# Kernel optimization log

Hardware: AMD Instinct MI355X
Metric: run time of the kernel (lower is better)

## Reference

```python
import jax, jax.numpy as jnp
import numpy as np

N_NODES = 20000
N_EDGES = 320000
DIM_IN = 768
DIM_H = 512
S_HOPS = 3
NUM_GNNS = 4
NEG_SLOPE = 0.2  # DGL GATConv default


def setup_inputs() -> dict:
    key = jax.random.key(0)
    ks = jax.random.split(key, 12)
    feat = jax.random.normal(ks[0], (N_NODES, DIM_IN), dtype=jnp.float32)
    src = jax.random.randint(ks[1], (N_EDGES,), 0, N_NODES)
    dst = jax.random.randint(ks[2], (N_EDGES,), 0, N_NODES)
    # learned params
    fc_W = jax.random.normal(ks[3], (DIM_IN, DIM_H), dtype=jnp.float32) * 0.02
    fc_b = jnp.zeros((DIM_H,), dtype=jnp.float32)
    gat_W = jax.random.normal(ks[4], (NUM_GNNS, DIM_H, DIM_H), dtype=jnp.float32) * 0.02
    gat_al = jax.random.normal(ks[5], (NUM_GNNS, DIM_H), dtype=jnp.float32) * 0.1
    gat_ar = jax.random.normal(ks[6], (NUM_GNNS, DIM_H), dtype=jnp.float32) * 0.1
    gat_b = jnp.zeros((NUM_GNNS, DIM_H), dtype=jnp.float32)
    beta = jnp.ones((S_HOPS + 1,), dtype=jnp.float32)
    return {"feat": feat, "fc_W": fc_W, "fc_b": fc_b, "gat_W": gat_W,
            "gat_al": gat_al, "gat_ar": gat_ar, "gat_b": gat_b,
            "beta": beta, "src": src, "dst": dst}


def _gat_layer(h, W, a_l, a_r, b, src, dst):
    z = h @ W                                   # [N, DH]
    el = z @ a_l                                # [N]
    er = z @ a_r                                # [N]
    e = jax.nn.leaky_relu(el[src] + er[dst], NEG_SLOPE)  # [E]
    # edge softmax over incoming edges of each dst node
    m = jax.ops.segment_max(e, dst, num_segments=N_NODES)
    ex = jnp.exp(e - m[dst])
    denom = jax.ops.segment_sum(ex, dst, num_segments=N_NODES)
    alpha = ex / denom[dst]                     # [E]
    out = jax.ops.segment_sum(alpha[:, None] * z[src], dst, num_segments=N_NODES)
    return out + b


def reference(feat, fc_W, fc_b, gat_W, gat_al, gat_ar, gat_b, beta, src, dst):
    h = feat @ fc_W + fc_b                      # dim_in -> 512
    for l in range(NUM_GNNS):
        h = _gat_layer(h, gat_W[l], gat_al[l], gat_ar[l], gat_b[l], src, dst)
    # A_hat = A + I propagation; A_hat @ Z = scatter(Z[src] -> dst) + Z
    Z_prev = h
    Z = beta[0] * Z_prev                        # accumulated Z is computed but the
    for s in range(1, S_HOPS + 1):              # original module returns Z_prev
        Z_s = jax.ops.segment_sum(Z_prev[src], dst, num_segments=N_NODES) + Z_prev
        Z = Z + beta[s] * Z_s
        Z_prev = Z_s
    return Z_prev
```

## Files before the change

kernel.cpp:

```cpp
#include <hip/hip_runtime.h>
#include <math.h>

#define N_NODES 20000
#define M_PAD   20096
#define N_EDGES 320000
#define DIM_IN 768
#define DIM_H 512
#define NUM_GNNS 4
#define NEG_SLOPE 0.2f

#define GEMM_TILES 628
#define GEMM_GRID  632

typedef __attribute__((ext_vector_type(8))) short short8;
typedef __attribute__((ext_vector_type(4))) float f32x4;

#define GPTR(p) (const __attribute__((address_space(1))) void*)(p)
#define LPTR(p) (__attribute__((address_space(3))) void*)(p)

__device__ __forceinline__ float bf2f(unsigned int lo16) {
  return __uint_as_float(lo16 << 16);
}
__device__ __forceinline__ unsigned short f2bf(float f) {
  unsigned int u = __float_as_uint(f);
  u += 0x7FFFu + ((u >> 16) & 1u);
  return (unsigned short)(u >> 16);
}
__device__ __forceinline__ void unpack8(uint4 v, float* f) {
  f[0] = bf2f(v.x & 0xffffu); f[1] = bf2f(v.x >> 16);
  f[2] = bf2f(v.y & 0xffffu); f[3] = bf2f(v.y >> 16);
  f[4] = bf2f(v.z & 0xffffu); f[5] = bf2f(v.z >> 16);
  f[6] = bf2f(v.w & 0xffffu); f[7] = bf2f(v.w >> 16);
}
__device__ __forceinline__ uint4 pack8(const float* o) {
  uint4 pv;
  pv.x = (unsigned)f2bf(o[0]) | ((unsigned)f2bf(o[1]) << 16);
  pv.y = (unsigned)f2bf(o[2]) | ((unsigned)f2bf(o[3]) << 16);
  pv.z = (unsigned)f2bf(o[4]) | ((unsigned)f2bf(o[5]) << 16);
  pv.w = (unsigned)f2bf(o[6]) | ((unsigned)f2bf(o[7]) << 16);
  return pv;
}

__device__ __forceinline__ float waveReduceSum(float v) {
#pragma unroll
  for (int off = 32; off > 0; off >>= 1) v += __shfl_xor(v, off, 64);
  return v;
}
__device__ __forceinline__ float waveReduceMax(float v) {
#pragma unroll
  for (int off = 32; off > 0; off >>= 1) v = fmaxf(v, __shfl_xor(v, off, 64));
  return v;
}

__global__ __launch_bounds__(256) void gemm_mfma_bf16(
    const unsigned short* __restrict__ A,
    const unsigned short* __restrict__ Bt,
    const float* __restrict__ bias,
    unsigned short* __restrict__ Cbf,
    int K) {
  int bid = blockIdx.x;
  int tile = (bid & 7) * (GEMM_GRID / 8) + (bid >> 3);
  if (tile >= GEMM_TILES) return;
  int brow = tile >> 2;
  int bcol = tile & 3;

  __shared__ __align__(16) unsigned short As[128 * 32];
  __shared__ __align__(16) unsigned short Bs[128 * 32];
  int tid = threadIdx.x;
  int wave = tid >> 6, lane = tid & 63;
  int wm = wave >> 1, wn = wave & 1;

  int rl = lane >> 2;
  int kc = (lane & 3) ^ ((lane >> 3) & 3);
  int r0 = 32 * wave;
  const unsigned short* gA0 = A + (size_t)(brow * 128 + r0 + rl) * K + kc * 8;
  const unsigned short* gA1 = gA0 + (size_t)16 * K;
  const unsigned short* gB0 = Bt + (size_t)(bcol * 128 + r0 + rl) * K + kc * 8;
  const unsigned short* gB1 = gB0 + (size_t)16 * K;
  unsigned short* lA0 = As + r0 * 32;
  unsigned short* lA1 = As + (r0 + 16) * 32;
  unsigned short* lB0 = Bs + r0 * 32;
  unsigned short* lB1 = Bs + (r0 + 16) * 32;

  int mrow = lane & 15;
  int q = lane >> 4;
  int swz = (q ^ ((mrow >> 1) & 3)) * 8;
  const short8* ra = (const short8*)(As + (64 * wm + mrow) * 32 + swz);
  const short8* rb = (const short8*)(Bs + (64 * wn + mrow) * 32 + swz);

  f32x4 acc[4][4];
#pragma unroll
  for (int i = 0; i < 4; ++i)
#pragma unroll
    for (int j = 0; j < 4; ++j) acc[i][j] = (f32x4)(0.f);

  for (int k0 = 0; k0 < K; k0 += 32) {
    __syncthreads();
    __builtin_amdgcn_global_load_lds(GPTR(gA0 + k0), LPTR(lA0), 16, 0, 0);
    __builtin_amdgcn_global_load_lds(GPTR(gA1 + k0), LPTR(lA1), 16, 0, 0);
    __builtin_amdgcn_global_load_lds(GPTR(gB0 + k0), LPTR(lB0), 16, 0, 0);
    __builtin_amdgcn_global_load_lds(GPTR(gB1 + k0), LPTR(lB1), 16, 0, 0);
    __syncthreads();
    short8 a[4], b[4];
#pragma unroll
    for (int t = 0; t < 4; ++t) a[t] = ra[t * 64];
#pragma unroll
    for (int t = 0; t < 4; ++t) b[t] = rb[t * 64];
#pragma unroll
    for (int mt = 0; mt < 4; ++mt)
#pragma unroll
      for (int nt = 0; nt < 4; ++nt)
        acc[mt][nt] = __builtin_amdgcn_mfma_f32_16x16x32_bf16(a[mt], b[nt], acc[mt][nt], 0, 0, 0);
  }

  int colb = bcol * 128 + 64 * wn + (lane & 15);
  int rowb = brow * 128 + 64 * wm + 4 * q;
#pragma unroll
  for (int nt = 0; nt < 4; ++nt) {
    int col = colb + 16 * nt;
    float bv = bias ? bias[col] : 0.f;
#pragma unroll
    for (int mt = 0; mt < 4; ++mt) {
      int row = rowb + 16 * mt;
#pragma unroll
      for (int i = 0; i < 4; ++i)
        Cbf[(size_t)(row + i) * DIM_H + col] = f2bf(acc[mt][nt][i] + bv);
    }
  }
}

__global__ void convert_feat(const float* __restrict__ feat, unsigned short* __restrict__ Abf) {
  int t = blockIdx.x * blockDim.x + threadIdx.x;
  const int CHUNKS = M_PAD * DIM_IN / 8;
  if (t >= CHUNKS) return;
  int row = t / (DIM_IN / 8);
  uint4 o;
  if (row < N_NODES) {
    const float4* p = (const float4*)(feat + (size_t)t * 8);
    float4 x = p[0], y = p[1];
    o.x = (unsigned)f2bf(x.x) | ((unsigned)f2bf(x.y) << 16);
    o.y = (unsigned)f2bf(x.z) | ((unsigned)f2bf(x.w) << 16);
    o.z = (unsigned)f2bf(y.x) | ((unsigned)f2bf(y.y) << 16);
    o.w = (unsigned)f2bf(y.z) | ((unsigned)f2bf(y.w) << 16);
  } else {
    o = make_uint4(0, 0, 0, 0);
  }
  ((uint4*)Abf)[t] = o;
}

__global__ __launch_bounds__(256) void transpose_bf16(const float* __restrict__ in,
                                                      unsigned short* __restrict__ out,
                                                      int R, int C) {
  __shared__ float tile[32][33];
  int tx = threadIdx.x, ty = threadIdx.y;
  size_t base = (size_t)blockIdx.z * R * C;
  int r0 = blockIdx.x * 32, c0 = blockIdx.y * 32;
#pragma unroll
  for (int i = 0; i < 4; ++i) {
    int r = r0 + ty + i * 8;
    tile[ty + i * 8][tx] = in[base + (size_t)r * C + c0 + tx];
  }
  __syncthreads();
#pragma unroll
  for (int i = 0; i < 4; ++i) {
    int c = c0 + ty + i * 8;
    out[base + (size_t)c * R + r0 + tx] = f2bf(tile[tx][ty + i * 8]);
  }
}

__global__ void count_edges(const int* __restrict__ dst, int* __restrict__ counts) {
  int k = blockIdx.x * blockDim.x + threadIdx.x;
  if (k < N_EDGES) atomicAdd(&counts[dst[k]], 1);
}

__global__ __launch_bounds__(1024) void scan_kernel(const int* __restrict__ counts,
                                                    int* __restrict__ indptr) {
  __shared__ int part[1024];
  int tid = threadIdx.x;
  const int CH = (N_NODES + 1023) / 1024;
  int base = tid * CH;
  int s = 0;
  for (int i = 0; i < CH; ++i) {
    int idx = base + i;
    if (idx < N_NODES) s += counts[idx];
  }
  part[tid] = s;
  __syncthreads();
  for (int off = 1; off < 1024; off <<= 1) {
    int v = (tid >= off) ? part[tid - off] : 0;
    __syncthreads();
    part[tid] += v;
    __syncthreads();
  }
  int run = (tid == 0) ? 0 : part[tid - 1];
  for (int i = 0; i < CH; ++i) {
    int idx = base + i;
    if (idx < N_NODES) {
      indptr[idx] = run;
      run += counts[idx];
      if (idx == N_NODES - 1) indptr[N_NODES] = run;
    }
  }
}

__global__ void fill_adj(const int* __restrict__ src, const int* __restrict__ dst,
                         const int* __restrict__ indptr, int* __restrict__ cursor,
                         int* __restrict__ adjsrc) {
  int k = blockIdx.x * blockDim.x + threadIdx.x;
  if (k < N_EDGES) {
    int d = dst[k];
    int pos = atomicAdd(&cursor[d], 1);
    adjsrc[indptr[d] + pos] = src[k];
  }
}

__global__ __launch_bounds__(256) void eler_bf(const unsigned short* __restrict__ zbf,
                                               const float* __restrict__ al,
                                               const float* __restrict__ ar,
                                               float* __restrict__ el, float* __restrict__ er) {
  int wid = (blockIdx.x * blockDim.x + threadIdx.x) >> 6;
  int lane = threadIdx.x & 63;
  if (wid >= N_NODES) return;
  uint4 zv = ((const uint4*)(zbf + (size_t)wid * DIM_H))[lane];
  float z[8];
  unpack8(zv, z);
  const float4* al4 = (const float4*)(al + lane * 8);
  const float4* ar4 = (const float4*)(ar + lane * 8);
  float4 a0 = al4[0], a1 = al4[1], r0 = ar4[0], r1 = ar4[1];
  float sl = z[0] * a0.x + z[1] * a0.y + z[2] * a0.z + z[3] * a0.w +
             z[4] * a1.x + z[5] * a1.y + z[6] * a1.z + z[7] * a1.w;
  float sr = z[0] * r0.x + z[1] * r0.y + z[2] * r0.z + z[3] * r0.w +
             z[4] * r1.x + z[5] * r1.y + z[6] * r1.z + z[7] * r1.w;
  sl = waveReduceSum(sl);
  sr = waveReduceSum(sr);
  if (lane == 0) { el[wid] = sl; er[wid] = sr; }
}

__global__ __launch_bounds__(256) void gat_aggregate_bf(
    const unsigned short* __restrict__ zbf, const float* __restrict__ el,
    const float* __restrict__ er, const int* __restrict__ indptr,
    const int* __restrict__ adjsrc, const float* __restrict__ bias,
    unsigned short* __restrict__ out_bf) {
  int v = (blockIdx.x * blockDim.x + threadIdx.x) >> 6;
  int lane = threadIdx.x & 63;
  if (v >= N_NODES) return;
  int begin = indptr[v], end = indptr[v + 1];
  float er_v = er[v];

  float m = -INFINITY;
  for (int j = begin + lane; j < end; j += 64) {
    float e = el[adjsrc[j]] + er_v;
    e = (e >= 0.f) ? e : NEG_SLOPE * e;
    m = fmaxf(m, e);
  }
  m = waveReduceMax(m);

  float ssum = 0.f;
  for (int j = begin + lane; j < end; j += 64) {
    float e = el[adjsrc[j]] + er_v;
    e = (e >= 0.f) ? e : NEG_SLOPE * e;
    ssum += __expf(e - m);
  }
  float denom = waveReduceSum(ssum);
  float inv = (end > begin) ? 1.f / denom : 0.f;

  float acc[8] = {};
  for (int c = begin; c < end; c += 64) {
    int cc = min(64, end - c);
    int has = (c + lane < end);
    int sIdx = has ? adjsrc[c + lane] : 0;
    float e = has ? el[sIdx] + er_v : 0.f;
    e = (e >= 0.f) ? e : NEG_SLOPE * e;
    float wl = has ? __expf(e - m) * inv : 0.f;
    int t = 0;
    for (; t + 4 <= cc; t += 4) {
      int s0 = __shfl(sIdx, t + 0), s1 = __shfl(sIdx, t + 1);
      int s2 = __shfl(sIdx, t + 2), s3 = __shfl(sIdx, t + 3);
      float w0 = __shfl(wl, t + 0), w1 = __shfl(wl, t + 1);
      float w2 = __shfl(wl, t + 2), w3 = __shfl(wl, t + 3);
      uint4 z0 = ((const uint4*)(zbf + (size_t)s0 * DIM_H))[lane];
      uint4 z1 = ((const uint4*)(zbf + (size_t)s1 * DIM_H))[lane];
      uint4 z2 = ((const uint4*)(zbf + (size_t)s2 * DIM_H))[lane];
      uint4 z3 = ((const uint4*)(zbf + (size_t)s3 * DIM_H))[lane];
      float f0[8], f1[8], f2[8], f3[8];
      unpack8(z0, f0); unpack8(z1, f1); unpack8(z2, f2); unpack8(z3, f3);
#pragma unroll
      for (int i = 0; i < 8; ++i)
        acc[i] += w0 * f0[i] + w1 * f1[i] + w2 * f2[i] + w3 * f3[i];
    }
    for (; t < cc; ++t) {
      int s0 = __shfl(sIdx, t);
      float w0 = __shfl(wl, t);
      uint4 z0 = ((const uint4*)(zbf + (size_t)s0 * DIM_H))[lane];
      float f0[8];
      unpack8(z0, f0);
#pragma unroll
      for (int i = 0; i < 8; ++i) acc[i] += w0 * f0[i];
    }
  }
  const float4* b4 = (const float4*)(bias + lane * 8);
  float4 b0 = b4[0], b1 = b4[1];
  float o[8] = {acc[0] + b0.x, acc[1] + b0.y, acc[2] + b0.z, acc[3] + b0.w,
                acc[4] + b1.x, acc[5] + b1.y, acc[6] + b1.z, acc[7] + b1.w};
  ((uint4*)(out_bf + (size_t)v * DIM_H))[lane] = pack8(o);
}

__global__ __launch_bounds__(256) void propagate_bf(const unsigned short* __restrict__ zin,
                                                    const int* __restrict__ indptr,
                                                    const int* __restrict__ adjsrc,
                                                    unsigned short* __restrict__ out_bf,
                                                    float* __restrict__ out_f32) {
  int v = (blockIdx.x * blockDim.x + threadIdx.x) >> 6;
  int lane = threadIdx.x & 63;
  if (v >= N_NODES) return;
  uint4 sv = ((const uint4*)(zin + (size_t)v * DIM_H))[lane];
  float acc[8];
  unpack8(sv, acc);
  int begin = indptr[v], end = indptr[v + 1];
  for (int c = begin; c < end; c += 64) {
    int cc = min(64, end - c);
    int sIdx = (c + lane < end) ? adjsrc[c + lane] : 0;
    int t = 0;
    for (; t + 4 <= cc; t += 4) {
      int s0 = __shfl(sIdx, t + 0), s1 = __shfl(sIdx, t + 1);
      int s2 = __shfl(sIdx, t + 2), s3 = __shfl(sIdx, t + 3);
      uint4 z0 = ((const uint4*)(zin + (size_t)s0 * DIM_H))[lane];
      uint4 z1 = ((const uint4*)(zin + (size_t)s1 * DIM_H))[lane];
      uint4 z2 = ((const uint4*)(zin + (size_t)s2 * DIM_H))[lane];
      uint4 z3 = ((const uint4*)(zin + (size_t)s3 * DIM_H))[lane];
      float f0[8], f1[8], f2[8], f3[8];
      unpack8(z0, f0); unpack8(z1, f1); unpack8(z2, f2); unpack8(z3, f3);
#pragma unroll
      for (int i = 0; i < 8; ++i) acc[i] += f0[i] + f1[i] + f2[i] + f3[i];
    }
    for (; t < cc; ++t) {
      int s0 = __shfl(sIdx, t);
      uint4 z0 = ((const uint4*)(zin + (size_t)s0 * DIM_H))[lane];
      float f0[8];
      unpack8(z0, f0);
#pragma unroll
      for (int i = 0; i < 8; ++i) acc[i] += f0[i];
    }
  }
  if (out_bf) {
    ((uint4*)(out_bf + (size_t)v * DIM_H))[lane] = pack8(acc);
  } else {
    float4* fr = (float4*)(out_f32 + (size_t)v * DIM_H + lane * 8);
    fr[0] = make_float4(acc[0], acc[1], acc[2], acc[3]);
    fr[1] = make_float4(acc[4], acc[5], acc[6], acc[7]);
  }
}

extern "C" void kernel_launch(void* const* d_in, const int* in_sizes, int n_in,
                              void* d_out, int out_size, void* d_ws, size_t ws_size,
                              hipStream_t stream) {
  const float* feat = (const float*)d_in[0];
  const float* fc_W = (const float*)d_in[1];
  const float* fc_b = (const float*)d_in[2];
  const float* gat_W = (const float*)d_in[3];
  const float* gat_al = (const float*)d_in[4];
  const float* gat_ar = (const float*)d_in[5];
  const float* gat_b = (const float*)d_in[6];
  const int* src = (const int*)d_in[8];
  const int* dst = (const int*)d_in[9];
  float* out = (float*)d_out;

  char* w = (char*)d_ws;
  auto alloc = [&](size_t bytes) {
    char* p = w;
    w += (bytes + 255) & ~(size_t)255;
    return p;
  };
  unsigned short* hbf   = (unsigned short*)alloc((size_t)M_PAD * DIM_H * 2);
  unsigned short* fcWt  = (unsigned short*)alloc((size_t)DIM_H * DIM_IN * 2);
  unsigned short* gatWt = (unsigned short*)alloc((size_t)NUM_GNNS * DIM_H * DIM_H * 2);
  float* el    = (float*)alloc((size_t)N_NODES * 4);
  float* er    = (float*)alloc((size_t)N_NODES * 4);
  int* counts  = (int*)alloc((size_t)2 * N_NODES * 4);
  int* cursor  = counts + N_NODES;
  int* indptr  = (int*)alloc((size_t)(N_NODES + 1) * 4);
  int* adjsrc  = (int*)alloc((size_t)N_EDGES * 4);
  char* uni = alloc((size_t)M_PAD * DIM_IN * 2);
  unsigned short* Abf = (unsigned short*)uni;
  unsigned short* Z1  = (unsigned short*)uni;
  unsigned short* zbf = (unsigned short*)d_out;

  hipMemsetAsync(counts, 0, sizeof(int) * 2 * N_NODES, stream);
  count_edges<<<(N_EDGES + 255) / 256, 256, 0, stream>>>(dst, counts);
  scan_kernel<<<1, 1024, 0, stream>>>(counts, indptr);
  fill_adj<<<(N_EDGES + 255) / 256, 256, 0, stream>>>(src, dst, indptr, cursor, adjsrc);

  convert_feat<<<(M_PAD * DIM_IN / 8 + 255) / 256, 256, 0, stream>>>(feat, Abf);
  transpose_bf16<<<dim3(DIM_IN / 32, DIM_H / 32, 1), dim3(32, 8), 0, stream>>>(fc_W, fcWt, DIM_IN, DIM_H);
  transpose_bf16<<<dim3(DIM_H / 32, DIM_H / 32, NUM_GNNS), dim3(32, 8), 0, stream>>>(gat_W, gatWt, DIM_H, DIM_H);

  gemm_mfma_bf16<<<GEMM_GRID, 256, 0, stream>>>(Abf, fcWt, fc_b, hbf, DIM_IN);

  int nwaveblocks = (N_NODES * 64 + 255) / 256;
  for (int l = 0; l < NUM_GNNS; ++l) {
    gemm_mfma_bf16<<<GEMM_GRID, 256, 0, stream>>>(hbf, gatWt + (size_t)l * DIM_H * DIM_H,
                                                  nullptr, zbf, DIM_H);
    eler_bf<<<nwaveblocks, 256, 0, stream>>>(zbf, gat_al + (size_t)l * DIM_H,
                                             gat_ar + (size_t)l * DIM_H, el, er);
    gat_aggregate_bf<<<nwaveblocks, 256, 0, stream>>>(
        zbf, el, er, indptr, adjsrc, gat_b + (size_t)l * DIM_H, hbf);
  }

  propagate_bf<<<nwaveblocks, 256, 0, stream>>>(hbf, indptr, adjsrc, Z1, nullptr);
  propagate_bf<<<nwaveblocks, 256, 0, stream>>>(Z1, indptr, adjsrc, hbf, nullptr);
  propagate_bf<<<nwaveblocks, 256, 0, stream>>>(hbf, indptr, adjsrc, nullptr, out);
}
```

Baseline: 636.5 us.

## Slice gather aggregation by column blocks and precompute edge softmax weights

Splits the GAT edge softmax into its own kernel that writes per-edge alpha to a buffer, then aggregates and propagates with a column-sliced layout. Each block now owns one 64-column slice of 4 nodes, and its 4 lane-groups each handle a different edge before a cross-slot shuffle reduction. Grouping blocks by slice is meant to improve cache locality of the gathered rows and raise parallelism for each node. In exchange it launches an extra kernel per layer, launches 8x more blocks, and makes smaller 8-byte gathers.

```diff
diff --git a/kernel.cpp b/kernel.cpp
--- a/kernel.cpp
+++ b/kernel.cpp
@@ -11,6 +11,9 @@
 
 #define GEMM_TILES 628
 #define GEMM_GRID  632
+
+#define NODE_WAVE_BLOCKS 5000
+#define SLICED_GRID (NODE_WAVE_BLOCKS * 8)
 
 typedef __attribute__((ext_vector_type(8))) short short8;
 typedef __attribute__((ext_vector_type(4))) float f32x4;
@@ -236,11 +239,10 @@
   if (lane == 0) { el[wid] = sl; er[wid] = sr; }
 }
 
-__global__ __launch_bounds__(256) void gat_aggregate_bf(
-    const unsigned short* __restrict__ zbf, const float* __restrict__ el,
-    const float* __restrict__ er, const int* __restrict__ indptr,
-    const int* __restrict__ adjsrc, const float* __restrict__ bias,
-    unsigned short* __restrict__ out_bf) {
+__global__ __launch_bounds__(256) void edge_softmax_alpha(
+    const float* __restrict__ el, const float* __restrict__ er,
+    const int* __restrict__ indptr, const int* __restrict__ adjsrc,
+    float* __restrict__ alpha) {
   int v = (blockIdx.x * blockDim.x + threadIdx.x) >> 6;
   int lane = threadIdx.x & 63;
   if (v >= N_NODES) return;
@@ -255,99 +257,142 @@
   }
   m = waveReduceMax(m);
 
-  float ssum = 0.f;
+  float ss = 0.f;
   for (int j = begin + lane; j < end; j += 64) {
     float e = el[adjsrc[j]] + er_v;
     e = (e >= 0.f) ? e : NEG_SLOPE * e;
-    ssum += __expf(e - m);
-  }
-  float denom = waveReduceSum(ssum);
+    ss += __expf(e - m);
+  }
+  float denom = waveReduceSum(ss);
   float inv = (end > begin) ? 1.f / denom : 0.f;
 
-  float acc[8] = {};
+  for (int j = begin + lane; j < end; j += 64) {
+    float e = el[adjsrc[j]] + er_v;
+    e = (e >= 0.f) ? e : NEG_SLOPE * e;
+    alpha[j] = __expf(e - m) * inv;
+  }
+}
+
+__global__ __launch_bounds__(256) void gat_aggregate_sliced(
+    const unsigned short* __restrict__ zbf, const float* __restrict__ alpha,
+    const int* __restrict__ indptr, const int* __restrict__ adjsrc,
+    const float* __restrict__ bias, unsigned short* __restrict__ out_bf) {
+  int slice = blockIdx.x & 7;
+  int group = blockIdx.x >> 3;
+  int wave = threadIdx.x >> 6, lane = threadIdx.x & 63;
+  int v = group * 4 + wave;
+  if (v >= N_NODES) return;
+  int slot = lane >> 4, sub = lane & 15;
+  int col = slice * 64 + sub * 4;
+  const unsigned short* zc = zbf + col;
+
+  int begin = indptr[v], end = indptr[v + 1];
+  float acc[4] = {0.f, 0.f, 0.f, 0.f};
+
   for (int c = begin; c < end; c += 64) {
     int cc = min(64, end - c);
-    int has = (c + lane < end);
-    int sIdx = has ? adjsrc[c + lane] : 0;
-    float e = has ? el[sIdx] + er_v : 0.f;
-    e = (e >= 0.f) ? e : NEG_SLOPE * e;
-    float wl = has ? __expf(e - m) * inv : 0.f;
+    bool has = (c + lane < end);
+    int idx = has ? adjsrc[c + lane] : 0;
+    float wv = has ? alpha[c + lane] : 0.f;
     int t = 0;
-    for (; t + 4 <= cc; t += 4) {
-      int s0 = __shfl(sIdx, t + 0), s1 = __shfl(sIdx, t + 1);
-      int s2 = __shfl(sIdx, t + 2), s3 = __shfl(sIdx, t + 3);
-      float w0 = __shfl(wl, t + 0), w1 = __shfl(wl, t + 1);
-      float w2 = __shfl(wl, t + 2), w3 = __shfl(wl, t + 3);
-      uint4 z0 = ((const uint4*)(zbf + (size_t)s0 * DIM_H))[lane];
-      uint4 z1 = ((const uint4*)(zbf + (size_t)s1 * DIM_H))[lane];
-      uint4 z2 = ((const uint4*)(zbf + (size_t)s2 * DIM_H))[lane];
-      uint4 z3 = ((const uint4*)(zbf + (size_t)s3 * DIM_H))[lane];
-      float f0[8], f1[8], f2[8], f3[8];
-      unpack8(z0, f0); unpack8(z1, f1); unpack8(z2, f2); unpack8(z3, f3);
-#pragma unroll
-      for (int i = 0; i < 8; ++i)
-        acc[i] += w0 * f0[i] + w1 * f1[i] + w2 * f2[i] + w3 * f3[i];
-    }
-    for (; t < cc; ++t) {
-      int s0 = __shfl(sIdx, t);
-      float w0 = __shfl(wl, t);
-      uint4 z0 = ((const uint4*)(zbf + (size_t)s0 * DIM_H))[lane];
-      float f0[8];
-      unpack8(z0, f0);
-#pragma unroll
-      for (int i = 0; i < 8; ++i) acc[i] += w0 * f0[i];
-    }
-  }
-  const float4* b4 = (const float4*)(bias + lane * 8);
-  float4 b0 = b4[0], b1 = b4[1];
-  float o[8] = {acc[0] + b0.x, acc[1] + b0.y, acc[2] + b0.z, acc[3] + b0.w,
-                acc[4] + b1.x, acc[5] + b1.y, acc[6] + b1.z, acc[7] + b1.w};
-  ((uint4*)(out_bf + (size_t)v * DIM_H))[lane] = pack8(o);
-}
-
-__global__ __launch_bounds__(256) void propagate_bf(const unsigned short* __restrict__ zin,
-                                                    const int* __restrict__ indptr,
-                                                    const int* __restrict__ adjsrc,
-                                                    unsigned short* __restrict__ out_bf,
-                                                    float* __restrict__ out_f32) {
-  int v = (blockIdx.x * blockDim.x + threadIdx.x) >> 6;
-  int lane = threadIdx.x & 63;
+    for (; (t + 2) * 4 <= cc; t += 2) {
+      int e0 = t * 4 + slot, e1 = e0 + 4;
+      int s0 = __shfl(idx, e0, 64), s1 = __shfl(idx, e1, 64);
+      float w0 = __shfl(wv, e0, 64), w1 = __shfl(wv, e1, 64);
+      uint2 z0 = *(const uint2*)(zc + (size_t)s0 * DIM_H);
+      uint2 z1 = *(const uint2*)(zc + (size_t)s1 * DIM_H);
+      acc[0] += w0 * bf2f(z0.x & 0xffffu) + w1 * bf2f(z1.x & 0xffffu);
+      acc[1] += w0 * bf2f(z0.x >> 16)     + w1 * bf2f(z1.x >> 16);
+      acc[2] += w0 * bf2f(z0.y & 0xffffu) + w1 * bf2f(z1.y & 0xffffu);
+      acc[3] += w0 * bf2f(z0.y >> 16)     + w1 * bf2f(z1.y >> 16);
+    }
+    for (; t * 4 < cc; ++t) {
+      int e0 = t * 4 + slot;
+      int s0 = __shfl(idx, e0, 64);
+      float w0 = __shfl(wv, e0, 64);
+      uint2 z0 = *(const uint2*)(zc + (size_t)s0 * DIM_H);
+      acc[0] += w0 * bf2f(z0.x & 0xffffu);
+      acc[1] += w0 * bf2f(z0.x >> 16);
+      acc[2] += w0 * bf2f(z0.y & 0xffffu);
+      acc[3] += w0 * bf2f(z0.y >> 16);
+    }
+  }
+#pragma unroll
+  for (int i = 0; i < 4; ++i) {
+    acc[i] += __shfl_xor(acc[i], 16, 64);
+    acc[i] += __shfl_xor(acc[i], 32, 64);
+  }
+  if (slot == 0) {
+    float4 bv = *(const float4*)(bias + col);
+    unsigned long long pv =
+        (unsigned long long)((unsigned)f2bf(acc[0] + bv.x) | ((unsigned)f2bf(acc[1] + bv.y) << 16)) |
+        ((unsigned long long)((unsigned)f2bf(acc[2] + bv.z) | ((unsigned)f2bf(acc[3] + bv.w) << 16)) << 32);
+    __builtin_nontemporal_store(pv, (unsigned long long*)(out_bf + (size_t)v * DIM_H + col));
+  }
+}
+
+__global__ __launch_bounds__(256) void propagate_sliced(
+    const unsigned short* __restrict__ zin, const int* __restrict__ indptr,
+    const int* __restrict__ adjsrc, unsigned short* __restrict__ out_bf,
+    float* __restrict__ out_f32) {
+  int slice = blockIdx.x & 7;
+  int group = blockIdx.x >> 3;
+  int wave = threadIdx.x >> 6, lane = threadIdx.x & 63;
+  int v = group * 4 + wave;
   if (v >= N_NODES) return;
-  uint4 sv = ((const uint4*)(zin + (size_t)v * DIM_H))[lane];
-  float acc[8];
-  unpack8(sv, acc);
+  int slot = lane >> 4, sub = lane & 15;
+  int col = slice * 64 + sub * 4;
+  const unsigned short* zc = zin + col;
+
   int begin = indptr[v], end = indptr[v + 1];
+  float acc[4] = {0.f, 0.f, 0.f, 0.f};
+  if (slot == 0) {
+    uint2 sv = *(const uint2*)(zc + (size_t)v * DIM_H);
+    acc[0] = bf2f(sv.x & 0xffffu); acc[1] = bf2f(sv.x >> 16);
+    acc[2] = bf2f(sv.y & 0xffffu); acc[3] = bf2f(sv.y >> 16);
+  }
+
   for (int c = begin; c < end; c += 64) {
     int cc = min(64, end - c);
-    int sIdx = (c + lane < end) ? adjsrc[c + lane] : 0;
+    int idx = (c + lane < end) ? adjsrc[c + lane] : 0;
     int t = 0;
-    for (; t + 4 <= cc; t += 4) {
-      int s0 = __shfl(sIdx, t + 0), s1 = __shfl(sIdx, t + 1);
-      int s2 = __shfl(sIdx, t + 2), s3 = __shfl(sIdx, t + 3);
-      uint4 z0 = ((const uint4*)(zin + (size_t)s0 * DIM_H))[lane];
-      uint4 z1 = ((const uint4*)(zin + (size_t)s1 * DIM_H))[lane];
-      uint4 z2 = ((const uint4*)(zin + (size_t)s2 * DIM_H))[lane];
-      uint4 z3 = ((const uint4*)(zin + (size_t)s3 * DIM_H))[lane];
-      float f0[8], f1[8], f2[8], f3[8];
-      unpack8(z0, f0); unpack8(z1, f1); unpack8(z2, f2); unpack8(z3, f3);
-#pragma unroll
-      for (int i = 0; i < 8; ++i) acc[i] += f0[i] + f1[i] + f2[i] + f3[i];
-    }
-    for (; t < cc; ++t) {
-      int s0 = __shfl(sIdx, t);
-      uint4 z0 = ((const uint4*)(zin + (size_t)s0 * DIM_H))[lane];
-      float f0[8];
-      unpack8(z0, f0);
-#pragma unroll
-      for (int i = 0; i < 8; ++i) acc[i] += f0[i];
-    }
-  }
-  if (out_bf) {
-    ((uint4*)(out_bf + (size_t)v * DIM_H))[lane] = pack8(acc);
-  } else {
-    float4* fr = (float4*)(out_f32 + (size_t)v * DIM_H + lane * 8);
-    fr[0] = make_float4(acc[0], acc[1], acc[2], acc[3]);
-    fr[1] = make_float4(acc[4], acc[5], acc[6], acc[7]);
+    for (; (t + 2) * 4 <= cc; t += 2) {
+      int e0 = t * 4 + slot, e1 = e0 + 4;
+      int s0 = __shfl(idx, e0, 64), s1 = __shfl(idx, e1, 64);
+      uint2 z0 = *(const uint2*)(zc + (size_t)s0 * DIM_H);
+      uint2 z1 = *(const uint2*)(zc + (size_t)s1 * DIM_H);
+      acc[0] += bf2f(z0.x & 0xffffu) + bf2f(z1.x & 0xffffu);
+      acc[1] += bf2f(z0.x >> 16)     + bf2f(z1.x >> 16);
+      acc[2] += bf2f(z0.y & 0xffffu) + bf2f(z1.y & 0xffffu);
+      acc[3] += bf2f(z0.y >> 16)     + bf2f(z1.y >> 16);
+    }
+    for (; t * 4 < cc; ++t) {
+      int e0 = t * 4 + slot;
+      int s0 = __shfl(idx, e0, 64);
+      if (e0 < cc) {
+        uint2 z0 = *(const uint2*)(zc + (size_t)s0 * DIM_H);
+        acc[0] += bf2f(z0.x & 0xffffu);
+        acc[1] += bf2f(z0.x >> 16);
+        acc[2] += bf2f(z0.y & 0xffffu);
+        acc[3] += bf2f(z0.y >> 16);
+      }
+    }
+  }
+#pragma unroll
+  for (int i = 0; i < 4; ++i) {
+    acc[i] += __shfl_xor(acc[i], 16, 64);
+    acc[i] += __shfl_xor(acc[i], 32, 64);
+  }
+  if (slot == 0) {
+    if (out_bf) {
+      unsigned long long pv =
+          (unsigned long long)((unsigned)f2bf(acc[0]) | ((unsigned)f2bf(acc[1]) << 16)) |
+          ((unsigned long long)((unsigned)f2bf(acc[2]) | ((unsigned)f2bf(acc[3]) << 16)) << 32);
+      __builtin_nontemporal_store(pv, (unsigned long long*)(out_bf + (size_t)v * DIM_H + col));
+    } else {
+      f32x4 fv = {acc[0], acc[1], acc[2], acc[3]};
+      __builtin_nontemporal_store(fv, (f32x4*)(out_f32 + (size_t)v * DIM_H + col));
+    }
   }
 }
 
@@ -382,6 +427,7 @@
   int* adjsrc  = (int*)alloc((size_t)N_EDGES * 4);
   char* uni = alloc((size_t)M_PAD * DIM_IN * 2);
   unsigned short* Abf = (unsigned short*)uni;
+  float* alpha = (float*)uni;
   unsigned short* Z1  = (unsigned short*)uni;
   unsigned short* zbf = (unsigned short*)d_out;
 
@@ -402,11 +448,12 @@
                                                   nullptr, zbf, DIM_H);
     eler_bf<<<nwaveblocks, 256, 0, stream>>>(zbf, gat_al + (size_t)l * DIM_H,
                                              gat_ar + (size_t)l * DIM_H, el, er);
-    gat_aggregate_bf<<<nwaveblocks, 256, 0, stream>>>(
-        zbf, el, er, indptr, adjsrc, gat_b + (size_t)l * DIM_H, hbf);
-  }
-
-  propagate_bf<<<nwaveblocks, 256, 0, stream>>>(hbf, indptr, adjsrc, Z1, nullptr);
-  propagate_bf<<<nwaveblocks, 256, 0, stream>>>(Z1, indptr, adjsrc, hbf, nullptr);
-  propagate_bf<<<nwaveblocks, 256, 0, stream>>>(hbf, indptr, adjsrc, nullptr, out);
-}
+    edge_softmax_alpha<<<nwaveblocks, 256, 0, stream>>>(el, er, indptr, adjsrc, alpha);
+    gat_aggregate_sliced<<<SLICED_GRID, 256, 0, stream>>>(
+        zbf, alpha, indptr, adjsrc, gat_b + (size_t)l * DIM_H, hbf);
+  }
+
+  propagate_sliced<<<SLICED_GRID, 256, 0, stream>>>(hbf, indptr, adjsrc, Z1, nullptr);
+  propagate_sliced<<<SLICED_GRID, 256, 0, stream>>>(Z1, indptr, adjsrc, hbf, nullptr);
+  propagate_sliced<<<SLICED_GRID, 256, 0, stream>>>(hbf, indptr, adjsrc, nullptr, out);
+}
```

Measured after the change: 742.9 us. +16.7%, slower.
